# Kernel optimization log

Measured on AMD Instinct MI355X. Metric: run time of the kernel, lower is better.

Reference implementation:

```python
import jax, jax.numpy as jnp
import numpy as np

N_HEADS = 16

def _apply_rope(x, cos, sin):
    # x: [B, S, H, D]; cos/sin: [S, D//2]
    B, S, H, D = x.shape
    half = D // 2
    x1, x2 = x[..., :half], x[..., half:]
    c = cos[:S, None, :]  # [S, 1, half] -> broadcast over heads
    s = sin[:S, None, :]
    o1 = x1 * c - x2 * s
    o2 = x1 * s + x2 * c
    return jnp.concatenate([o1, o2], axis=-1).astype(x.dtype)


def setup_inputs() -> dict:
    key = jax.random.key(0)
    ks = jax.random.split(key, 6)
    B, S, dim = 2, 2048, 2048
    head_dim = dim // N_HEADS
    half = head_dim // 2
    x = jax.random.normal(ks[0], (B, S, dim), dtype=jnp.float32)
    # real RoPE tables (theta=10000)
    inv_freq = 1.0 / (10000.0 ** (np.arange(0, half, dtype=np.float32) / half))
    t = np.arange(S, dtype=np.float32)
    freqs = np.outer(t, inv_freq)  # [S, half]
    cos = jnp.asarray(np.cos(freqs), dtype=jnp.float32)
    sin = jnp.asarray(np.sin(freqs), dtype=jnp.float32)
    scale = 0.02
    wq = jax.random.normal(ks[1], (dim, dim), dtype=jnp.float32) * scale
    wk = jax.random.normal(ks[2], (dim, dim), dtype=jnp.float32) * scale
    wv = jax.random.normal(ks[3], (dim, dim), dtype=jnp.float32) * scale
    wo = jax.random.normal(ks[4], (dim, dim), dtype=jnp.float32) * scale
    return {"x": x, "cos": cos, "sin": sin, "wq": wq, "wk": wk, "wv": wv, "wo": wo}


def reference(x, cos, sin, wq, wk, wv, wo):
    B, S, dim = x.shape
    H = N_HEADS
    Dh = dim // H
    # QKV projections (nn.Linear: x @ W.T)
    q = (x @ wq.T).reshape(B, S, H, Dh)
    k = (x @ wk.T).reshape(B, S, H, Dh)
    v = (x @ wv.T).reshape(B, S, H, Dh)
    q = _apply_rope(q, cos, sin)
    k = _apply_rope(k, cos, sin)
    # causal attention (flash_attn_func with causal=True, dropout 0 in eval)
    scores = jnp.einsum('bqhd,bkhd->bhqk', q, k) / jnp.sqrt(jnp.asarray(Dh, x.dtype))
    causal = jnp.tril(jnp.ones((S, S), dtype=bool))
    scores = jnp.where(causal, scores, jnp.asarray(-1e30, x.dtype))
    attn = jax.nn.softmax(scores, axis=-1)
    out = jnp.einsum('bhqk,bkhd->bqhd', attn, v).reshape(B, S, dim)
    return out @ wo.T
```

## Files before the change

kernel.cpp:

```cpp
#include <hip/hip_runtime.h>

typedef short short8 __attribute__((ext_vector_type(8)));
typedef float f32x4 __attribute__((ext_vector_type(4)));
typedef unsigned short ushort_t;

__device__ __forceinline__ unsigned short f2bf(float f){
  unsigned int u = __builtin_bit_cast(unsigned int, f);
  u += 0x7FFFu + ((u >> 16) & 1u);
  return (unsigned short)(u >> 16);
}
__device__ __forceinline__ float bf2f(unsigned short u){
  return __builtin_bit_cast(float, ((unsigned int)u) << 16);
}
__device__ __forceinline__ void gload_lds16(const void* g, void* l){
  __builtin_amdgcn_global_load_lds((const __attribute__((address_space(1))) unsigned int*)g,
                                   (__attribute__((address_space(3))) unsigned int*)l, 16, 0, 0);
}

__global__ __launch_bounds__(256) void cast_bf16_kernel(const float* __restrict__ in,
                                                        ushort_t* __restrict__ out, long n4){
  long i = (long)blockIdx.x*256 + threadIdx.x;
  if (i >= n4) return;
  const float4 v = reinterpret_cast<const float4*>(in)[i];
  ushort4 o; o.x=f2bf(v.x); o.y=f2bf(v.y); o.z=f2bf(v.z); o.w=f2bf(v.w);
  reinterpret_cast<ushort4*>(out)[i] = o;
}

__global__ __launch_bounds__(256) void cast4_bf16_kernel(const float* __restrict__ w0, const float* __restrict__ w1,
                                                         const float* __restrict__ w2, const float* __restrict__ w3,
                                                         ushort_t* __restrict__ o0, ushort_t* __restrict__ o1,
                                                         ushort_t* __restrict__ o2, ushort_t* __restrict__ o3,
                                                         long n4){
  long i = (long)blockIdx.x*256 + threadIdx.x;
  if (i >= n4) return;
  const float* in; ushort_t* out;
  switch (blockIdx.y){
    case 0: in = w0; out = o0; break;
    case 1: in = w1; out = o1; break;
    case 2: in = w2; out = o2; break;
    default: in = w3; out = o3; break;
  }
  const float4 v = reinterpret_cast<const float4*>(in)[i];
  ushort4 o; o.x=f2bf(v.x); o.y=f2bf(v.y); o.z=f2bf(v.z); o.w=f2bf(v.w);
  reinterpret_cast<ushort4*>(out)[i] = o;
}

__global__ __launch_bounds__(256) void rope_kernel(const ushort_t* __restrict__ X,
                                                   const float* __restrict__ cosb,
                                                   const float* __restrict__ sinb,
                                                   ushort_t* __restrict__ Out, float scale){
  long idx = (long)blockIdx.x*256 + threadIdx.x;
  int dq = (int)(idx & 15);
  long rest = idx >> 4;
  int h = (int)(rest & 15); rest >>= 4;
  int s = (int)(rest & 2047);
  int b = (int)(rest >> 11);
  long base = ((long)(b*2048 + s))*2048 + h*128;
  int d0 = dq*4;
  ushort4 x1 = *(const ushort4*)&X[base + d0];
  ushort4 x2 = *(const ushort4*)&X[base + 64 + d0];
  float4 cc = *(const float4*)&cosb[s*64 + d0];
  float4 ss = *(const float4*)&sinb[s*64 + d0];
  ushort4 o1, o2;
  { float a=bf2f(x1.x), bb=bf2f(x2.x); o1.x=f2bf((a*cc.x-bb*ss.x)*scale); o2.x=f2bf((a*ss.x+bb*cc.x)*scale); }
  { float a=bf2f(x1.y), bb=bf2f(x2.y); o1.y=f2bf((a*cc.y-bb*ss.y)*scale); o2.y=f2bf((a*ss.y+bb*cc.y)*scale); }
  { float a=bf2f(x1.z), bb=bf2f(x2.z); o1.z=f2bf((a*cc.z-bb*ss.z)*scale); o2.z=f2bf((a*ss.z+bb*cc.z)*scale); }
  { float a=bf2f(x1.w), bb=bf2f(x2.w); o1.w=f2bf((a*cc.w-bb*ss.w)*scale); o2.w=f2bf((a*ss.w+bb*cc.w)*scale); }
  *(ushort4*)&Out[base + d0] = o1;
  *(ushort4*)&Out[base + 64 + d0] = o2;
}

__global__ __launch_bounds__(256) void vt_kernel(const ushort_t* __restrict__ vf,
                                                 ushort_t* __restrict__ vt){
  const int s0 = blockIdx.x*64;
  const int bh = blockIdx.y;
  const int b = bh >> 4, h = bh & 15;
  const int tid = threadIdx.x;
  __shared__ ushort_t tile[128][72];
#pragma unroll
  for (int i = 0; i < 4; ++i){
    int q = i*256 + tid;
    int sl = q >> 4, dc = (q & 15)*8;
    short8 v = *(const short8*)&vf[((long)(b*2048 + s0 + sl))*2048 + h*128 + dc];
#pragma unroll
    for (int k = 0; k < 8; ++k) tile[dc + k][sl] = (ushort_t)v[k];
  }
  __syncthreads();
#pragma unroll
  for (int i = 0; i < 4; ++i){
    int q = i*256 + tid;
    int d = q >> 3, sc = (q & 7)*8;
    *(short8*)&vt[((long)(bh*128 + d))*2048 + s0 + sc] = *(const short8*)&tile[d][sc];
  }
}

template<typename CT>
__global__ __launch_bounds__(256) void gemm_nt_lds(const ushort_t* __restrict__ A,
                                                   const ushort_t* __restrict__ B,
                                                   CT* __restrict__ C,
                                                   int M, int N, int K){
  const int tid = threadIdx.x;
  const int l = tid & 63;
  const int g = l >> 4, c = l & 15;
  const int w = tid >> 6, wr = w >> 1, wc = w & 1;
  const long m0 = (long)blockIdx.x*128, n0 = (long)blockIdx.y*128;
  __shared__ ushort_t lds_a[128*32];
  __shared__ ushort_t lds_b[128*32];
  f32x4 acc[4][4] = {};
  const int q1 = tid, q2 = 256 + tid;
  const ushort_t* a1 = A + (m0 + (q1>>2))*(long)K + (q1&3)*8;
  const ushort_t* a2 = A + (m0 + (q2>>2))*(long)K + (q2&3)*8;
  const ushort_t* b1 = B + (n0 + (q1>>2))*(long)K + (q1&3)*8;
  const ushort_t* b2 = B + (n0 + (q2>>2))*(long)K + (q2&3)*8;
  for (int k0 = 0; k0 < K; k0 += 32){
    __syncthreads();
    gload_lds16(a1 + k0, &lds_a[q1*8]);
    gload_lds16(a2 + k0, &lds_a[q2*8]);
    gload_lds16(b1 + k0, &lds_b[q1*8]);
    gload_lds16(b2 + k0, &lds_b[q2*8]);
    __syncthreads();
    short8 af[4], bf[4];
#pragma unroll
    for (int i = 0; i < 4; ++i) af[i] = *(const short8*)&lds_a[(wr*64 + i*16 + c)*32 + g*8];
#pragma unroll
    for (int j = 0; j < 4; ++j) bf[j] = *(const short8*)&lds_b[(wc*64 + j*16 + c)*32 + g*8];
#pragma unroll
    for (int i = 0; i < 4; ++i)
#pragma unroll
      for (int j = 0; j < 4; ++j)
        acc[i][j] = __builtin_amdgcn_mfma_f32_16x16x32_bf16(af[i], bf[j], acc[i][j], 0, 0, 0);
  }
#pragma unroll
  for (int i = 0; i < 4; ++i)
#pragma unroll
    for (int j = 0; j < 4; ++j)
#pragma unroll
      for (int r = 0; r < 4; ++r){
        long off = (m0 + wr*64 + i*16 + g*4 + r)*(long)N + n0 + wc*64 + j*16 + c;
        if constexpr (sizeof(CT) == 2) C[off] = (CT)f2bf(acc[i][j][r]);
        else                           C[off] = acc[i][j][r];
      }
}

__global__ __launch_bounds__(256) void attn_kernel(const ushort_t* __restrict__ Q,
                                                   const ushort_t* __restrict__ Kr,
                                                   const ushort_t* __restrict__ Vt,
                                                   ushort_t* __restrict__ O){
  const int tid = threadIdx.x;
  const int l = tid & 63, w = tid >> 6;
  const int g = l >> 4, c = l & 15;
  const int bh = blockIdx.x;
  const int qt = (int)gridDim.y - 1 - (int)blockIdx.y;
  const int b = bh >> 4, h = bh & 15;
  const int q0 = qt * 64;
  const int qw0 = q0 + w * 16;
  const int nt = qt + 1;

  __shared__ ushort_t k_lds[2][64*128];
  __shared__ ushort_t v_lds[2][128*64];
  __shared__ ushort_t p_lds[4][16*72];

  short8 qf[4];
  const long qbase = ((long)(b*2048 + qw0 + c))*2048 + h*128 + g*8;
#pragma unroll
  for (int ds = 0; ds < 4; ++ds) qf[ds] = *(const short8*)(Q + qbase + ds*32);

  const ushort_t* ksrc[4]; const ushort_t* vsrc[4];
  int kof[4], vof[4];
#pragma unroll
  for (int i = 0; i < 4; ++i){
    int q = i*256 + tid;
    int r = q >> 4, j = q & 15;
    ksrc[i] = Kr + ((long)(b*2048 + r))*2048 + h*128 + (j ^ (r & 7))*8;
    kof[i] = q*8;
    int d = q >> 3, jj = q & 7;
    vsrc[i] = Vt + ((long)(bh*128 + d))*2048 + (jj ^ (d & 7))*8;
    vof[i] = q*8;
  }

  f32x4 o[8] = {};
  float m = -1e30f, lsum = 0.f;
  const int sw = (c & 7) << 3;

#pragma unroll
  for (int i = 0; i < 4; ++i) gload_lds16(ksrc[i], &k_lds[0][kof[i]]);
#pragma unroll
  for (int i = 0; i < 4; ++i) gload_lds16(vsrc[i], &v_lds[0][vof[i]]);
  __syncthreads();

  for (int t = 0; t < nt; ++t){
    const int p = t & 1;
    if (t + 1 < nt){
#pragma unroll
      for (int i = 0; i < 4; ++i)
        gload_lds16(ksrc[i] + (long)(t+1)*64*2048, &k_lds[p^1][kof[i]]);
#pragma unroll
      for (int i = 0; i < 4; ++i)
        gload_lds16(vsrc[i] + (t+1)*64, &v_lds[p^1][vof[i]]);
    }
    const int kv0 = t*64;

    f32x4 s[4] = {};
    __builtin_amdgcn_s_setprio(1);
#pragma unroll
    for (int t4 = 0; t4 < 4; ++t4){
      const int row = 16*t4 + c;
#pragma unroll
      for (int ds = 0; ds < 4; ++ds){
        short8 kf = *(const short8*)&k_lds[p][(row*128 + ds*32 + g*8) ^ sw];
        s[t4] = __builtin_amdgcn_mfma_f32_16x16x32_bf16(kf, qf[ds], s[t4], 0, 0, 0);
      }
    }
    __builtin_amdgcn_s_setprio(0);
    if (kv0 + 63 > qw0){
      const int qg = qw0 + c;
#pragma unroll
      for (int t4 = 0; t4 < 4; ++t4)
#pragma unroll
        for (int r = 0; r < 4; ++r)
          if (kv0 + 16*t4 + 4*g + r > qg) s[t4][r] = -1e30f;
    }
    float tm = -1e30f;
#pragma unroll
    for (int t4 = 0; t4 < 4; ++t4)
      tm = fmaxf(tm, fmaxf(fmaxf(s[t4][0], s[t4][1]), fmaxf(s[t4][2], s[t4][3])));
    tm = fmaxf(tm, __shfl_xor(tm, 16, 64));
    tm = fmaxf(tm, __shfl_xor(tm, 32, 64));
    float mn = fmaxf(m, tm);
    float al = __expf(m - mn);
    float ps = 0.f;
#pragma unroll
    for (int t4 = 0; t4 < 4; ++t4)
#pragma unroll
      for (int r = 0; r < 4; ++r){ float pex = __expf(s[t4][r] - mn); s[t4][r] = pex; ps += pex; }
    ps += __shfl_xor(ps, 16, 64);
    ps += __shfl_xor(ps, 32, 64);
    lsum = lsum*al + ps;
    m = mn;
    float alr[4];
#pragma unroll
    for (int r = 0; r < 4; ++r) alr[r] = __shfl(al, 4*g + r, 64);
#pragma unroll
    for (int dt = 0; dt < 8; ++dt)
#pragma unroll
      for (int r = 0; r < 4; ++r) o[dt][r] *= alr[r];
#pragma unroll
    for (int t4 = 0; t4 < 4; ++t4){
      uint2 pw;
      pw.x = (unsigned)f2bf(s[t4][0]) | ((unsigned)f2bf(s[t4][1]) << 16);
      pw.y = (unsigned)f2bf(s[t4][2]) | ((unsigned)f2bf(s[t4][3]) << 16);
      *reinterpret_cast<uint2*>(&p_lds[w][c*72 + 16*t4 + 4*g]) = pw;
    }
    __builtin_amdgcn_s_setprio(1);
#pragma unroll
    for (int kc = 0; kc < 2; ++kc){
      short8 pf = *(const short8*)&p_lds[w][c*72 + 32*kc + 8*g];
#pragma unroll
      for (int dt = 0; dt < 8; ++dt){
        short8 vf = *(const short8*)&v_lds[p][(((16*dt + c)*64) + kc*32 + g*8) ^ sw];
        o[dt] = __builtin_amdgcn_mfma_f32_16x16x32_bf16(pf, vf, o[dt], 0, 0, 0);
      }
    }
    __builtin_amdgcn_s_setprio(0);
    __syncthreads();
  }

  float inv = 1.f / lsum;
  float invr[4];
#pragma unroll
  for (int r = 0; r < 4; ++r) invr[r] = __shfl(inv, 4*g + r, 64);
  const long obase = ((long)(b*2048 + qw0 + g*4))*2048 + h*128 + c;
#pragma unroll
  for (int dt = 0; dt < 8; ++dt)
#pragma unroll
    for (int r = 0; r < 4; ++r)
      O[obase + (long)r*2048 + dt*16] = f2bf(o[dt][r] * invr[r]);
}

extern "C" void kernel_launch(void* const* d_in, const int* in_sizes, int n_in,
                              void* d_out, int out_size, void* d_ws, size_t ws_size,
                              hipStream_t stream){
  const float* x    = (const float*)d_in[0];
  const float* cosb = (const float*)d_in[1];
  const float* sinb = (const float*)d_in[2];
  const float* wq   = (const float*)d_in[3];
  const float* wk   = (const float*)d_in[4];
  const float* wv   = (const float*)d_in[5];
  const float* wo   = (const float*)d_in[6];
  float* out = (float*)d_out;

  const int S = 2048, DIM = 2048;
  const long MN = 4096;

  char* ws = (char*)d_ws;
  ushort_t* xb    = (ushort_t*)(ws);
  ushort_t* wqb   = (ushort_t*)(ws + (16l<<20));
  ushort_t* wkb   = (ushort_t*)(ws + (24l<<20));
  ushort_t* wvb   = (ushort_t*)(ws + (32l<<20));
  ushort_t* wob   = (ushort_t*)(ws + (40l<<20));
  ushort_t* stage = (ushort_t*)(ws + (48l<<20));
  ushort_t* attnb = (ushort_t*)(ws + (64l<<20));
  ushort_t* qr    = (ushort_t*)(ws + (80l<<20));
  ushort_t* kr    = (ushort_t*)(ws + (96l<<20));
  ushort_t* vt    = (ushort_t*)(ws + (112l<<20));

  const long xn4 = MN*DIM/4, wn4 = (long)DIM*DIM/4;
  cast_bf16_kernel<<<(int)((xn4+255)/256), 256, 0, stream>>>(x, xb, xn4);
  cast4_bf16_kernel<<<dim3((int)((wn4+255)/256), 4), 256, 0, stream>>>(
      wq, wk, wv, wo, wqb, wkb, wvb, wob, wn4);

  dim3 ggrid(MN/128, DIM/128);
  const int ropeBlocks = (2*2048*16*16)/256;

  gemm_nt_lds<ushort_t><<<ggrid, 256, 0, stream>>>(xb, wqb, stage, (int)MN, DIM, DIM);
  rope_kernel<<<ropeBlocks, 256, 0, stream>>>(stage, cosb, sinb, qr, 0.08838834764831845f);
  gemm_nt_lds<ushort_t><<<ggrid, 256, 0, stream>>>(xb, wkb, stage, (int)MN, DIM, DIM);
  rope_kernel<<<ropeBlocks, 256, 0, stream>>>(stage, cosb, sinb, kr, 1.0f);
  gemm_nt_lds<ushort_t><<<ggrid, 256, 0, stream>>>(xb, wvb, stage, (int)MN, DIM, DIM);
  vt_kernel<<<dim3(S/64, 32), 256, 0, stream>>>(stage, vt);
  attn_kernel<<<dim3(32, S/64), 256, 0, stream>>>(qr, kr, vt, attnb);
  gemm_nt_lds<float><<<ggrid, 256, 0, stream>>>(attnb, wob, out, (int)MN, DIM, DIM);
}
```

Baseline: 330.8 us.

## Fuse QKV projections into one pipelined 256x256 GEMM, batch RoPE, lazy softmax rescale

Concatenates the Q, K and V weights and replaces three separate 128x128 GEMMs with a single 256x256-tile, 512-thread GEMM. That GEMM uses an 8-phase double-buffered LDS pipeline, XOR-swizzled LDS and an XCD-aware block remap, and writes Q, K and V into separate staging buffers. The two RoPE launches become one in-place launch over a 2D grid. The attention softmax skips the running-max rescale of the output accumulator unless the tile max exceeds the old max by more than 8, which removes exp and multiply work but lets intermediate values grow up to about e^8 before correction.

```diff
diff --git a/kernel.cpp b/kernel.cpp
--- a/kernel.cpp
+++ b/kernel.cpp
@@ -45,11 +45,13 @@
   reinterpret_cast<ushort4*>(out)[i] = o;
 }
 
-__global__ __launch_bounds__(256) void rope_kernel(const ushort_t* __restrict__ X,
-                                                   const float* __restrict__ cosb,
-                                                   const float* __restrict__ sinb,
-                                                   ushort_t* __restrict__ Out, float scale){
+__global__ __launch_bounds__(256) void rope2_kernel(ushort_t* __restrict__ Qs,
+                                                    ushort_t* __restrict__ Ks,
+                                                    const float* __restrict__ cosb,
+                                                    const float* __restrict__ sinb){
   long idx = (long)blockIdx.x*256 + threadIdx.x;
+  ushort_t* X = blockIdx.y ? Ks : Qs;
+  const float scale = blockIdx.y ? 1.0f : 0.08838834764831845f;
   int dq = (int)(idx & 15);
   long rest = idx >> 4;
   int h = (int)(rest & 15); rest >>= 4;
@@ -66,8 +68,8 @@
   { float a=bf2f(x1.y), bb=bf2f(x2.y); o1.y=f2bf((a*cc.y-bb*ss.y)*scale); o2.y=f2bf((a*ss.y+bb*cc.y)*scale); }
   { float a=bf2f(x1.z), bb=bf2f(x2.z); o1.z=f2bf((a*cc.z-bb*ss.z)*scale); o2.z=f2bf((a*ss.z+bb*cc.z)*scale); }
   { float a=bf2f(x1.w), bb=bf2f(x2.w); o1.w=f2bf((a*cc.w-bb*ss.w)*scale); o2.w=f2bf((a*ss.w+bb*cc.w)*scale); }
-  *(ushort4*)&Out[base + d0] = o1;
-  *(ushort4*)&Out[base + 64 + d0] = o2;
+  *(ushort4*)&X[base + d0] = o1;
+  *(ushort4*)&X[base + 64 + d0] = o2;
 }
 
 __global__ __launch_bounds__(256) void vt_kernel(const ushort_t* __restrict__ vf,
@@ -94,10 +96,122 @@
   }
 }
 
-template<typename CT>
+
+#define LDA8(P, QM) do{ \
+  _Pragma("unroll") for (int i_ = 0; i_ < 4; ++i_){ \
+    af[i_][0] = *(const short8*)&lA[(P)*16384 + ((QM)*128 + aRowBase + i_*16)*64 + sw0]; \
+    af[i_][1] = *(const short8*)&lA[(P)*16384 + ((QM)*128 + aRowBase + i_*16)*64 + sw1]; } }while(0)
+
+#define LDB4(P, QN) do{ \
+  _Pragma("unroll") for (int j_ = 0; j_ < 2; ++j_){ \
+    bfr[j_][0] = *(const short8*)&lB[(P)*16384 + ((QN)*128 + bRowBase + j_*16)*64 + sw0]; \
+    bfr[j_][1] = *(const short8*)&lB[(P)*16384 + ((QN)*128 + bRowBase + j_*16)*64 + sw1]; } }while(0)
+
+#define STAGE_A(P, QM, T) do{ \
+  gload_lds16(aS0 + (long)(QM)*64*K + (long)(T)*64, &lA[(P)*16384 + (QM)*8192 + tid*8]); \
+  gload_lds16(aS1 + (long)(QM)*64*K + (long)(T)*64, &lA[(P)*16384 + (QM)*8192 + 4096 + tid*8]); }while(0)
+
+#define STAGE_B(P, QN, T) do{ \
+  gload_lds16(bS0 + (long)(QN)*32*K + (long)(T)*64, &lB[(P)*16384 + (QN)*8192 + tid*8]); \
+  gload_lds16(bS1 + (long)(QN)*32*K + (long)(T)*64, &lB[(P)*16384 + (QN)*8192 + 4096 + tid*8]); }while(0)
+
+#define MF16(QM, QN) do{ \
+  __builtin_amdgcn_s_setprio(1); \
+  _Pragma("unroll") for (int i_ = 0; i_ < 4; ++i_){ \
+    _Pragma("unroll") for (int j_ = 0; j_ < 2; ++j_){ \
+      acc[(QM)*4+i_][(QN)*2+j_] = __builtin_amdgcn_mfma_f32_16x16x32_bf16(af[i_][0], bfr[j_][0], acc[(QM)*4+i_][(QN)*2+j_], 0, 0, 0); \
+      acc[(QM)*4+i_][(QN)*2+j_] = __builtin_amdgcn_mfma_f32_16x16x32_bf16(af[i_][1], bfr[j_][1], acc[(QM)*4+i_][(QN)*2+j_], 0, 0, 0); } } \
+  __builtin_amdgcn_s_setprio(0); }while(0)
+
+#define WAITC(MORE) do{ \
+  if (MORE) asm volatile("s_waitcnt vmcnt(4)" ::: "memory"); \
+  else      asm volatile("s_waitcnt vmcnt(0)" ::: "memory"); }while(0)
+
+#define PH(P, QM, QN, STG, WT) do{ \
+  if ((QN) == 0) { LDA8(P, QM); } \
+  LDB4(P, QN); \
+  STG; \
+  WT; \
+  __builtin_amdgcn_s_barrier(); \
+  asm volatile("" ::: "memory"); \
+  MF16(QM, QN); \
+  __builtin_amdgcn_s_barrier(); \
+  asm volatile("" ::: "memory"); }while(0)
+
+__global__ __launch_bounds__(512, 2) void gemm_qkv_8ph(const ushort_t* __restrict__ A,
+                                                       const ushort_t* __restrict__ Bw,
+                                                       ushort_t* __restrict__ Cq,
+                                                       int MT, int K){
+  __shared__ ushort_t lA[32768];
+  __shared__ ushort_t lB[32768];
+  const int tid = threadIdx.x;
+  const int lane = tid & 63, wid = tid >> 6;
+  const int g = lane >> 4, c = lane & 15;
+  const int wm = wid >> 2, wn = wid & 3;
+
+  const int nwg = (int)gridDim.x, cpx = nwg >> 3;
+  int sw = (blockIdx.x & 7)*cpx + (blockIdx.x >> 3);
+  const long m0 = (long)(sw % MT)*256;
+  const long n0 = (long)(sw / MT)*256;
+
+  const int prl0 = tid >> 3, q1 = 512 + tid, prl1 = q1 >> 3;
+  const int sl0 = ((tid & 7) ^ (prl0 & 7)) * 8;
+  const int sl1 = ((q1 & 7) ^ (prl1 & 7)) * 8;
+  const int rowA0 = ((prl0 >> 6)*128) + (prl0 & 63);
+  const int rowA1 = ((prl1 >> 6)*128) + (prl1 & 63);
+  const int rowB0 = ((prl0 >> 5)*64) + (prl0 & 31);
+  const int rowB1 = ((prl1 >> 5)*64) + (prl1 & 31);
+  const ushort_t* aS0 = A + (m0 + rowA0)*K + sl0;
+  const ushort_t* aS1 = A + (m0 + rowA1)*K + sl1;
+  const ushort_t* bS0 = Bw + (n0 + rowB0)*K + sl0;
+  const ushort_t* bS1 = Bw + (n0 + rowB1)*K + sl1;
+
+  const int sw0 = (g ^ (c & 7)) * 8;
+  const int sw1 = ((4 + g) ^ (c & 7)) * 8;
+  const int aRowBase = wm*64 + c;
+  const int bRowBase = wn*32 + c;
+
+  f32x4 acc[8][4] = {};
+  short8 af[4][2], bfr[2][2];
+  const int NI = K >> 7;
+
+  STAGE_A(0, 0, 0); STAGE_B(0, 0, 0);
+  STAGE_A(0, 1, 0); STAGE_B(0, 1, 0);
+  STAGE_A(1, 0, 1); STAGE_B(1, 0, 1);
+  asm volatile("s_waitcnt vmcnt(4)" ::: "memory");
+  __builtin_amdgcn_s_barrier();
+  asm volatile("" ::: "memory");
+
+  for (int j = 0; j < NI; ++j){
+    const int t = 2*j;
+    const bool more = (j + 1 < NI);
+    PH(0, 0, 0, STAGE_A(1, 1, t+1), ((void)0));
+    PH(0, 0, 1, STAGE_B(1, 1, t+1), ((void)0));
+    PH(0, 1, 0, if(more){STAGE_A(0, 0, t+2);}, ((void)0));
+    PH(0, 1, 1, if(more){STAGE_B(0, 0, t+2);}, WAITC(more));
+    PH(1, 0, 0, if(more){STAGE_A(0, 1, t+2);}, ((void)0));
+    PH(1, 0, 1, if(more){STAGE_B(0, 1, t+2);}, ((void)0));
+    PH(1, 1, 0, if(more){STAGE_A(1, 0, t+3);}, ((void)0));
+    PH(1, 1, 1, if(more){STAGE_B(1, 0, t+3);}, WAITC(more));
+  }
+
+  const long rbase = m0 + wm*128 + g*4;
+  const long cbase = n0 + wn*64 + c;
+#pragma unroll
+  for (int mi = 0; mi < 8; ++mi)
+#pragma unroll
+    for (int ni = 0; ni < 4; ++ni){
+      long col6 = cbase + ni*16;
+      long off = (long)(col6 >> 11)*8388608 + (rbase + mi*16)*2048 + (col6 & 2047);
+#pragma unroll
+      for (int r = 0; r < 4; ++r)
+        Cq[off + (long)r*2048] = f2bf(acc[mi][ni][r]);
+    }
+}
+
 __global__ __launch_bounds__(256) void gemm_nt_lds(const ushort_t* __restrict__ A,
                                                    const ushort_t* __restrict__ B,
-                                                   CT* __restrict__ C,
+                                                   float* __restrict__ C,
                                                    int M, int N, int K){
   const int tid = threadIdx.x;
   const int l = tid & 63;
@@ -135,11 +249,8 @@
 #pragma unroll
     for (int j = 0; j < 4; ++j)
 #pragma unroll
-      for (int r = 0; r < 4; ++r){
-        long off = (m0 + wr*64 + i*16 + g*4 + r)*(long)N + n0 + wc*64 + j*16 + c;
-        if constexpr (sizeof(CT) == 2) C[off] = (CT)f2bf(acc[i][j][r]);
-        else                           C[off] = acc[i][j][r];
-      }
+      for (int r = 0; r < 4; ++r)
+        C[(m0 + wr*64 + i*16 + g*4 + r)*(long)N + n0 + wc*64 + j*16 + c] = acc[i][j][r];
 }
 
 __global__ __launch_bounds__(256) void attn_kernel(const ushort_t* __restrict__ Q,
@@ -226,24 +337,27 @@
       tm = fmaxf(tm, fmaxf(fmaxf(s[t4][0], s[t4][1]), fmaxf(s[t4][2], s[t4][3])));
     tm = fmaxf(tm, __shfl_xor(tm, 16, 64));
     tm = fmaxf(tm, __shfl_xor(tm, 32, 64));
-    float mn = fmaxf(m, tm);
-    float al = __expf(m - mn);
+    if (!__all(tm <= m + 8.f)){
+      float mn = fmaxf(m, tm);
+      float al = __expf(m - mn);
+      m = mn;
+      lsum *= al;
+      float alr[4];
+#pragma unroll
+      for (int r = 0; r < 4; ++r) alr[r] = __shfl(al, 4*g + r, 64);
+#pragma unroll
+      for (int dt = 0; dt < 8; ++dt)
+#pragma unroll
+        for (int r = 0; r < 4; ++r) o[dt][r] *= alr[r];
+    }
     float ps = 0.f;
 #pragma unroll
     for (int t4 = 0; t4 < 4; ++t4)
 #pragma unroll
-      for (int r = 0; r < 4; ++r){ float pex = __expf(s[t4][r] - mn); s[t4][r] = pex; ps += pex; }
+      for (int r = 0; r < 4; ++r){ float pex = __expf(s[t4][r] - m); s[t4][r] = pex; ps += pex; }
     ps += __shfl_xor(ps, 16, 64);
     ps += __shfl_xor(ps, 32, 64);
-    lsum = lsum*al + ps;
-    m = mn;
-    float alr[4];
-#pragma unroll
-    for (int r = 0; r < 4; ++r) alr[r] = __shfl(al, 4*g + r, 64);
-#pragma unroll
-    for (int dt = 0; dt < 8; ++dt)
-#pragma unroll
-      for (int r = 0; r < 4; ++r) o[dt][r] *= alr[r];
+    lsum += ps;
 #pragma unroll
     for (int t4 = 0; t4 < 4; ++t4){
       uint2 pw;
@@ -293,31 +407,26 @@
   const long MN = 4096;
 
   char* ws = (char*)d_ws;
-  ushort_t* xb    = (ushort_t*)(ws);
-  ushort_t* wqb   = (ushort_t*)(ws + (16l<<20));
-  ushort_t* wkb   = (ushort_t*)(ws + (24l<<20));
-  ushort_t* wvb   = (ushort_t*)(ws + (32l<<20));
-  ushort_t* wob   = (ushort_t*)(ws + (40l<<20));
-  ushort_t* stage = (ushort_t*)(ws + (48l<<20));
-  ushort_t* attnb = (ushort_t*)(ws + (64l<<20));
-  ushort_t* qr    = (ushort_t*)(ws + (80l<<20));
-  ushort_t* kr    = (ushort_t*)(ws + (96l<<20));
-  ushort_t* vt    = (ushort_t*)(ws + (112l<<20));
+  ushort_t* xb     = (ushort_t*)(ws);
+  ushort_t* wqkvb  = (ushort_t*)(ws + (16l<<20));
+  ushort_t* wob    = (ushort_t*)(ws + (40l<<20));
+  ushort_t* qstage = (ushort_t*)(ws + (48l<<20));
+  ushort_t* kstage = (ushort_t*)(ws + (64l<<20));
+  ushort_t* vstage = (ushort_t*)(ws + (80l<<20));
+  ushort_t* vt     = (ushort_t*)(ws + (96l<<20));
+  ushort_t* attnb  = vstage;
 
   const long xn4 = MN*DIM/4, wn4 = (long)DIM*DIM/4;
   cast_bf16_kernel<<<(int)((xn4+255)/256), 256, 0, stream>>>(x, xb, xn4);
   cast4_bf16_kernel<<<dim3((int)((wn4+255)/256), 4), 256, 0, stream>>>(
-      wq, wk, wv, wo, wqb, wkb, wvb, wob, wn4);
-
-  dim3 ggrid(MN/128, DIM/128);
+      wq, wk, wv, wo,
+      wqkvb, wqkvb + 4194304, wqkvb + 8388608, wob, wn4);
+
+  gemm_qkv_8ph<<<(MN/256)*(6144/256), 512, 0, stream>>>(xb, wqkvb, qstage, (int)(MN/256), DIM);
+
   const int ropeBlocks = (2*2048*16*16)/256;
-
-  gemm_nt_lds<ushort_t><<<ggrid, 256, 0, stream>>>(xb, wqb, stage, (int)MN, DIM, DIM);
-  rope_kernel<<<ropeBlocks, 256, 0, stream>>>(stage, cosb, sinb, qr, 0.08838834764831845f);
-  gemm_nt_lds<ushort_t><<<ggrid, 256, 0, stream>>>(xb, wkb, stage, (int)MN, DIM, DIM);
-  rope_kernel<<<ropeBlocks, 256, 0, stream>>>(stage, cosb, sinb, kr, 1.0f);
-  gemm_nt_lds<ushort_t><<<ggrid, 256, 0, stream>>>(xb, wvb, stage, (int)MN, DIM, DIM);
-  vt_kernel<<<dim3(S/64, 32), 256, 0, stream>>>(stage, vt);
-  attn_kernel<<<dim3(32, S/64), 256, 0, stream>>>(qr, kr, vt, attnb);
-  gemm_nt_lds<float><<<ggrid, 256, 0, stream>>>(attnb, wob, out, (int)MN, DIM, DIM);
-}
+  rope2_kernel<<<dim3(ropeBlocks, 2), 256, 0, stream>>>(qstage, kstage, cosb, sinb);
+  vt_kernel<<<dim3(S/64, 32), 256, 0, stream>>>(vstage, vt);
+  attn_kernel<<<dim3(32, S/64), 256, 0, stream>>>(qstage, kstage, vt, attnb);
+  gemm_nt_lds<<<dim3(MN/128, DIM/128), 256, 0, stream>>>(attnb, wob, out, (int)MN, DIM, DIM);
+}
```

New measurement: 304.3 us. -8.0%, faster.
